# Performance work log

Hardware: AMD Instinct MI355X
Metric: run time of the kernel (lower is better)

## Reference

```python
import jax, jax.numpy as jnp
import numpy as np

B, N, DIM, H = 16, 1024, 512, 8
HEAD_DIM = DIM // H
SCALE = HEAD_DIM ** -0.5


def _dct_matrix(m):
    # Orthonormal DCT-II matrix, matching cv2.dct: D[0,:]=sqrt(1/m),
    # D[k,n]=sqrt(2/m)*cos(pi*(2n+1)*k/(2m)) for k>0.
    n = jnp.arange(m, dtype=jnp.float32)
    k = n[:, None]
    D = jnp.sqrt(2.0 / m) * jnp.cos(jnp.pi * (2.0 * n[None, :] + 1.0) * k / (2.0 * m))
    return D.at[0, :].set(jnp.sqrt(1.0 / m))


def setup_inputs() -> dict:
    key = jax.random.key(0)
    ks = jax.random.split(key, 9)
    def lin(k, fan_in, shape):
        return jax.random.normal(k, shape, jnp.float32) * (1.0 / np.sqrt(fan_in))
    return {
        "x": jax.random.normal(ks[0], (B, N, DIM), jnp.float32),
        "qkv_w": lin(ks[1], DIM, (DIM, 3 * DIM)),
        "qkv_b": lin(ks[2], DIM, (3 * DIM,)),
        "proj_w": lin(ks[3], DIM, (DIM, DIM)),
        "proj_b": lin(ks[4], DIM, (DIM,)),
        "h1_w": lin(ks[5], DIM, (DIM, DIM // 4)),
        "h1_b": jnp.zeros((DIM // 4,), jnp.float32),
        "h2_w": lin(ks[6], DIM // 4, (DIM // 4, H)),
        "h2_b": jnp.zeros((H,), jnp.float32),
        "freq_w": jnp.float32(0.5),
    }


def _extract_dct_features(x):
    # x: (B, N, C). Mirrors extract_dct_features incl. the .detach() in torch.
    B_, N_, _ = x.shape
    m = int(np.ceil(np.sqrt(N_)))  # static
    x_mean = x.mean(axis=-1)                                   # (B, N)
    A = jnp.pad(x_mean, ((0, 0), (0, m * m - N_))).reshape(B_, m, m)
    D = _dct_matrix(m)
    dct2 = jnp.einsum('km,bmn,ln->bkl', D, A, D)               # 2D DCT per sample
    dct_feat = dct2.reshape(B_, m * m)[:, :N_]
    dct_feat = jnp.clip(dct_feat, -10.0, 10.0)
    norm = jnp.linalg.norm(dct_feat, axis=1, keepdims=True) + 1e-5
    return jax.lax.stop_gradient(dct_feat / norm)              # (B, N)


def reference(x, qkv_w, qkv_b, proj_w, proj_b, h1_w, h1_b, h2_w, h2_b, freq_w):
    B_, N_, C = x.shape
    # QKV projection -> (3, B, H, N, head_dim)
    qkv = (x @ qkv_w + qkv_b).reshape(B_, N_, 3, H, C // H)
    qkv = jnp.transpose(qkv, (2, 0, 3, 1, 4))
    q, k, v = qkv[0] * SCALE, qkv[1], qkv[2]
    attn = jnp.einsum('bhnd,bhmd->bhnm', q, k)                 # (B, H, N, N)

    # Frequency-domain attention term
    dct_feat = _extract_dct_features(x)                        # (B, N)
    x_avg = x.mean(axis=1)                                     # (B, C)
    head_w = jax.nn.relu(x_avg @ h1_w + h1_b) @ h2_w + h2_b    # (B, H)
    weighted = dct_feat[:, None, :] * head_w[:, :, None]       # (B, H, N)
    freq_attn = jnp.einsum('bhn,bhm->bnm', weighted, weighted) # (B, N, N)
    row_sum = jnp.maximum(freq_attn.sum(axis=-1, keepdims=True), 1e-5)
    freq_attn = jnp.clip(freq_attn / row_sum, 0.0, 1.0)

    aw = jax.nn.sigmoid(freq_w)
    attn = (1.0 - aw) * attn + aw * freq_attn[:, None, :, :]
    attn = jax.nn.softmax(attn, axis=-1)

    out = jnp.einsum('bhnm,bhmd->bhnd', attn, v)
    out = jnp.transpose(out, (0, 2, 1, 3)).reshape(B_, N_, C)
    return out @ proj_w + proj_b
```

## Files before the change

kernel.cpp:

```cpp
#include <hip/hip_runtime.h>
#include <hip/hip_bf16.h>
#include <math.h>

#define PI_F  3.14159265358979323846f
#define LOG2E 1.44269504088896340736f

typedef __attribute__((ext_vector_type(8))) short          bf16x8;
typedef __attribute__((ext_vector_type(8))) unsigned short ushort8;
typedef __attribute__((ext_vector_type(4))) float          f32x4;

__device__ __forceinline__ unsigned short f2bf(float f) {
  union { float f; unsigned u; } v; v.f = f;
  unsigned r = v.u + 0x7fffu + ((v.u >> 16) & 1u);
  return (unsigned short)(r >> 16);
}

__device__ __forceinline__ unsigned short f2bf_hw(float f) {
  __hip_bfloat16 h = __float2bfloat16(f);
  return *reinterpret_cast<unsigned short*>(&h);
}

#define GLOAD16(g, l)                                                         \
  __builtin_amdgcn_global_load_lds(                                           \
      (const __attribute__((address_space(1))) void*)(g),                     \
      (__attribute__((address_space(3))) void*)(l), 16, 0, 0)

static const size_t OFF_XB  = 0;
static const size_t OFF_QB  = 16777216;
static const size_t OFF_KB  = 33554432;
static const size_t OFF_VT  = 67108864;
static const size_t OFF_AO  = 83886080;
static const size_t OFF_WT  = 100663296;
static const size_t OFF_PWT = 102236160;
static const size_t OFF_XM  = 102760448;
static const size_t OFF_XA  = 102825984;
static const size_t OFF_DF  = 102858752;
static const size_t OFF_CR  = 102924352;

__global__ __launch_bounds__(256) void k_xmean_cvt(const float* __restrict__ x,
                                                   float* __restrict__ xmean,
                                                   unsigned short* __restrict__ xb) {
  int row  = blockIdx.x * 4 + (threadIdx.x >> 6);
  int lane = threadIdx.x & 63;
  const float* px = x + (size_t)row * 512 + lane * 8;
  float4 a = ((const float4*)px)[0];
  float4 b = ((const float4*)px)[1];
  ushort8 o;
  o[0] = f2bf(a.x); o[1] = f2bf(a.y); o[2] = f2bf(a.z); o[3] = f2bf(a.w);
  o[4] = f2bf(b.x); o[5] = f2bf(b.y); o[6] = f2bf(b.z); o[7] = f2bf(b.w);
  *(ushort8*)(xb + (size_t)row * 512 + lane * 8) = o;
  float s = a.x + a.y + a.z + a.w + b.x + b.y + b.z + b.w;
  for (int off = 32; off; off >>= 1) s += __shfl_down(s, off);
  if (lane == 0) xmean[row] = s * (1.f / 512.f);
}

__global__ __launch_bounds__(512) void k_xavg(const unsigned short* __restrict__ xb,
                                              float* __restrict__ xavg) {
  int b = blockIdx.x, chunk = blockIdx.y;
  int c = threadIdx.x;
  const unsigned short* px = xb + ((size_t)b * 1024 + (size_t)chunk * 64) * 512 + c;
  float s = 0.f;
#pragma unroll 8
  for (int n = 0; n < 64; ++n) {
    unsigned u = (unsigned)px[(size_t)n * 512] << 16;
    s += *reinterpret_cast<float*>(&u);
  }
  atomicAdd(&xavg[b * 512 + c], s);
}

__global__ __launch_bounds__(1024) void k_dct_headw(const float* __restrict__ xmean,
                                                    const float* __restrict__ xavg,
                                                    const float* __restrict__ h1w,
                                                    const float* __restrict__ h1b,
                                                    const float* __restrict__ h2w,
                                                    const float* __restrict__ h2b,
                                                    const float* __restrict__ freqw,
                                                    float* __restrict__ dfeat,
                                                    float* __restrict__ crow) {
  __shared__ float A[32][33], Dm[32][33], Tm[32][33];
  __shared__ float red[1024];
  __shared__ float nrm, tsum_s;
  __shared__ float xa[512];
  __shared__ float part[8][128];
  __shared__ float h1s[128];
  __shared__ float hw[8];
  int b = blockIdx.x, t = threadIdx.x;
  if (t < 512) xa[t] = xavg[b * 512 + t] * (1.f / 1024.f);
  int kk = t >> 5, nn = t & 31;
  A[kk][nn] = xmean[b * 1024 + t];
  float dv = (kk == 0) ? sqrtf(1.f / 32.f)
                       : sqrtf(2.f / 32.f) * cosf(PI_F * (2.f * nn + 1.f) * (float)kk / 64.f);
  Dm[kk][nn] = dv;
  __syncthreads();
  float acc = 0.f;
  for (int m = 0; m < 32; ++m) acc += Dm[kk][m] * A[m][nn];
  Tm[kk][nn] = acc;
  __syncthreads();
  float acc2 = 0.f;
  for (int n = 0; n < 32; ++n) acc2 += Tm[kk][n] * Dm[nn][n];
  float val = fminf(fmaxf(acc2, -10.f), 10.f);
  red[t] = val * val;
  __syncthreads();
  for (int s = 512; s; s >>= 1) { if (t < s) red[t] += red[t + s]; __syncthreads(); }
  if (t == 0) nrm = sqrtf(red[0]) + 1e-5f;
  __syncthreads();
  float dn = val / nrm;
  dfeat[b * 1024 + t] = dn;
  red[t] = dn;
  __syncthreads();
  for (int s = 512; s; s >>= 1) { if (t < s) red[t] += red[t + s]; __syncthreads(); }
  if (t == 0) tsum_s = red[0];
  {
    int j = t & 127, c = t >> 7;
    float a1 = 0.f;
    const float* wcol = h1w + (size_t)c * 64 * 128 + j;
#pragma unroll 8
    for (int i = 0; i < 64; ++i) a1 += xa[c * 64 + i] * wcol[(size_t)i * 128];
    part[c][j] = a1;
  }
  __syncthreads();
  if (t < 128) {
    float a1 = h1b[t];
#pragma unroll
    for (int c = 0; c < 8; ++c) a1 += part[c][t];
    h1s[t] = fmaxf(a1, 0.f);
  }
  __syncthreads();
  if (t < 8) {
    float a2 = h2b[t];
    for (int j = 0; j < 128; ++j) a2 += h1s[j] * h2w[j * 8 + t];
    hw[t] = a2;
  }
  __syncthreads();
  float s2 = 0.f;
#pragma unroll
  for (int h = 0; h < 8; ++h) s2 += hw[h] * hw[h];
  float Tb = tsum_s;
  const float aw2 = (1.f / (1.f + __expf(-freqw[0]))) * LOG2E;
  float p = s2 * dn;
  crow[b * 1024 + t] = aw2 * p / fmaxf(p * Tb, 1e-5f);
}

__global__ __launch_bounds__(256) void k_wtrans2(const float* __restrict__ w1,
                                                 unsigned short* __restrict__ wt1,
                                                 const float* __restrict__ w2,
                                                 unsigned short* __restrict__ wt2) {
  __shared__ unsigned short T[64 * 65];
  int bx = blockIdx.x;
  const float* w;
  unsigned short* wt;
  int Nw, n0;
  if (bx < 24) { w = w1; wt = wt1; Nw = 1536; n0 = bx * 64; }
  else         { w = w2; wt = wt2; Nw = 512;  n0 = (bx - 24) * 64; }
  int k0 = blockIdx.y * 64;
  int t = threadIdx.x;
  int r = t >> 2, c0 = (t & 3) * 16;
  const float* src = w + (size_t)(k0 + r) * Nw + n0 + c0;
#pragma unroll
  for (int q = 0; q < 4; ++q) {
    float4 v4 = *(const float4*)(src + q * 4);
    T[(c0 + q * 4 + 0) * 65 + r] = f2bf(v4.x);
    T[(c0 + q * 4 + 1) * 65 + r] = f2bf(v4.y);
    T[(c0 + q * 4 + 2) * 65 + r] = f2bf(v4.z);
    T[(c0 + q * 4 + 3) * 65 + r] = f2bf(v4.w);
  }
  __syncthreads();
  int nl = t >> 2, koff = (t & 3) * 16;
  ushort8 o0, o1;
#pragma unroll
  for (int e = 0; e < 8; ++e) o0[e] = T[nl * 65 + koff + e];
#pragma unroll
  for (int e = 0; e < 8; ++e) o1[e] = T[nl * 65 + koff + 8 + e];
  unsigned short* dst = wt + (size_t)(n0 + nl) * 512 + k0 + koff;
  *(ushort8*)(dst) = o0;
  *(ushort8*)(dst + 8) = o1;
}

template <int MODE>
__global__ __launch_bounds__(256) void k_gemm(const unsigned short* __restrict__ A,
                                              const unsigned short* __restrict__ Bt,
                                              const float* __restrict__ bias,
                                              const float* __restrict__ freqw,
                                              unsigned short* __restrict__ o_q,
                                              unsigned short* __restrict__ o_k,
                                              unsigned short* __restrict__ o_vt,
                                              float* __restrict__ o_f) {
  __shared__ __align__(16) unsigned short As[128 * 64];
  __shared__ __align__(16) unsigned short Bs[128 * 64];
  const int t = threadIdx.x, w = t >> 6, l = t & 63;
  const int lg = l >> 4, ln = l & 15;
  const int wm = w >> 1, wn = w & 1;
  constexpr int NX = (MODE == 0) ? 12 : 4;
  const int bid = blockIdx.x, xcd = bid & 7, idx = bid >> 3;
  const int bx = idx % NX, by = xcd * 16 + idx / NX;
  const int row0 = by * 128, col0 = bx * 128;

  f32x4 acc[4][4];
#pragma unroll
  for (int i = 0; i < 4; ++i)
#pragma unroll
    for (int j = 0; j < 4; ++j) acc[i][j] = (f32x4){0.f, 0.f, 0.f, 0.f};

  int aoff[4][2], boff[4][2];
#pragma unroll
  for (int mt = 0; mt < 4; ++mt)
#pragma unroll
    for (int ks = 0; ks < 2; ++ks) {
      int ra = wm * 64 + mt * 16 + ln;
      aoff[mt][ks] = ra * 64 + (((lg + ks * 4) ^ (ra & 7)) << 3);
      int rb = wn * 64 + mt * 16 + ln;
      boff[mt][ks] = rb * 64 + (((lg + ks * 4) ^ (rb & 7)) << 3);
    }

  for (int k0 = 0; k0 < 512; k0 += 64) {
#pragma unroll
    for (int j = 0; j < 4; ++j) {
      int g = (j * 4 + w) * 64 + l;
      int row = g >> 3, slot = g & 7;
      int ss = slot ^ (row & 7);
      GLOAD16(A + (size_t)(row0 + row) * 512 + k0 + ss * 8, As + (size_t)(j * 4 + w) * 512);
      GLOAD16(Bt + (size_t)(col0 + row) * 512 + k0 + ss * 8, Bs + (size_t)(j * 4 + w) * 512);
    }
    __syncthreads();
#pragma unroll
    for (int ks = 0; ks < 2; ++ks) {
      bf16x8 av[4], bv[4];
#pragma unroll
      for (int mt = 0; mt < 4; ++mt) av[mt] = *(const bf16x8*)(As + aoff[mt][ks]);
#pragma unroll
      for (int nt = 0; nt < 4; ++nt) bv[nt] = *(const bf16x8*)(Bs + boff[nt][ks]);
#pragma unroll
      for (int mt = 0; mt < 4; ++mt)
#pragma unroll
        for (int nt = 0; nt < 4; ++nt)
          acc[mt][nt] = __builtin_amdgcn_mfma_f32_16x16x32_bf16(av[mt], bv[nt], acc[mt][nt], 0, 0, 0);
    }
    __syncthreads();
  }

  if (MODE == 0) {
    const int sel = col0 >> 9;
    if (sel == 2) {
      unsigned short* T = (wn == 0) ? As : Bs;
#pragma unroll
      for (int nt = 0; nt < 4; ++nt) {
        int dcol = nt * 16 + ln;
        float bcol = bias[col0 + wn * 64 + dcol];
#pragma unroll
        for (int mt = 0; mt < 4; ++mt)
#pragma unroll
          for (int r = 0; r < 4; ++r) {
            int rowL = wm * 64 + mt * 16 + lg * 4 + r;
            int slot = (rowL >> 3) ^ (dcol & 7);
            T[dcol * 128 + slot * 8 + (rowL & 7)] = f2bf(acc[mt][nt][r] + bcol);
          }
      }
      __syncthreads();
      int b_ = row0 >> 10, n0 = row0 & 1023;
      int h0 = (col0 & 511) >> 6;
      int dcol = t >> 2, rseg = (t & 3) * 32;
#pragma unroll
      for (int half = 0; half < 2; ++half) {
        const unsigned short* S = half ? Bs : As;
        size_t plane = ((size_t)(b_ * 8 + h0 + half)) << 16;
        unsigned short* dst = o_vt + plane + (size_t)dcol * 1024 + n0 + rseg;
#pragma unroll
        for (int j = 0; j < 4; ++j) {
          int slot = ((rseg >> 3) + j) ^ (dcol & 7);
          *(ushort8*)(dst + j * 8) = *(const ushort8*)(S + dcol * 128 + slot * 8);
        }
      }
      return;
    }
    unsigned short* outp = (sel == 0) ? o_q : o_k;
    const float aw = 1.f / (1.f + __expf(-freqw[0]));
    const float scl = (sel == 0) ? 0.125f * (1.f - aw) * LOG2E : 1.f;
#pragma unroll
    for (int nt = 0; nt < 4; ++nt) {
      int colg = col0 + wn * 64 + nt * 16 + ln;
      float bcol = bias[colg];
      int h = (colg >> 6) & 7, d = colg & 63;
#pragma unroll
      for (int mt = 0; mt < 4; ++mt)
#pragma unroll
        for (int r = 0; r < 4; ++r) {
          int row = row0 + wm * 64 + mt * 16 + lg * 4 + r;
          int bidx = row >> 10, n = row & 1023;
          float val = (acc[mt][nt][r] + bcol) * scl;
          outp[(((size_t)(bidx * 8 + h)) << 16) + (n << 6) + d] = f2bf(val);
        }
    }
  } else {
#pragma unroll
    for (int nt = 0; nt < 4; ++nt) {
      int colg = col0 + wn * 64 + nt * 16 + ln;
      float bcol = bias[colg];
#pragma unroll
      for (int mt = 0; mt < 4; ++mt)
#pragma unroll
        for (int r = 0; r < 4; ++r) {
          int row = row0 + wm * 64 + mt * 16 + lg * 4 + r;
          o_f[(size_t)row * 512 + colg] = acc[mt][nt][r] + bcol;
        }
    }
  }
}

__global__ __launch_bounds__(256) void k_attn(const unsigned short* __restrict__ qb,
                                              const unsigned short* __restrict__ kb,
                                              const unsigned short* __restrict__ vtg,
                                              const float* __restrict__ crow,
                                              const float* __restrict__ dfeat,
                                              const float* __restrict__ freqw,
                                              unsigned short* __restrict__ ao) {
  __shared__ __align__(16) unsigned short Ks[2][64 * 64];
  __shared__ __align__(16) unsigned short Vs[2][64 * 64];
  __shared__ __align__(16) unsigned short Ps[4][32 * 64];
  __shared__ __align__(16) float Df[1024];
  const int bid = blockIdx.x, xcd = bid & 7, idx = bid >> 3;
  const int bh = xcd * 16 + (idx >> 3), qt = idx & 7;
  const int b = bh >> 3, h = bh & 7;
  const int t = threadIdx.x, w = t >> 6, l = t & 63;
  const int lg = l >> 4, ln = l & 15;
  const size_t base = ((size_t)(b * 8 + h)) << 16;
  const float aw2 = (1.f / (1.f + __expf(-freqw[0]))) * LOG2E;

  *(float4*)(&Df[t * 4]) = *(const float4*)(dfeat + b * 1024 + t * 4);

  const int qrow0 = qt * 128 + w * 32;
  bf16x8 qf[2][2];
#pragma unroll
  for (int mt = 0; mt < 2; ++mt)
#pragma unroll
    for (int ks = 0; ks < 2; ++ks)
      qf[mt][ks] = *(const bf16x8*)(qb + base + (size_t)(qrow0 + mt * 16 + ln) * 64 + lg * 8 + ks * 32);

  float cr2[2][4];
#pragma unroll
  for (int mt = 0; mt < 2; ++mt)
#pragma unroll
    for (int r = 0; r < 4; ++r)
      cr2[mt][r] = crow[b * 1024 + qrow0 + mt * 16 + lg * 4 + r];

  f32x4 accO[2][4];
#pragma unroll
  for (int mt = 0; mt < 2; ++mt)
#pragma unroll
    for (int dt = 0; dt < 4; ++dt) accO[mt][dt] = (f32x4){0.f, 0.f, 0.f, 0.f};
  float mrow[2][4], psum[2][4];
#pragma unroll
  for (int mt = 0; mt < 2; ++mt)
#pragma unroll
    for (int r = 0; r < 4; ++r) { mrow[mt][r] = -1e30f; psum[mt][r] = 0.f; }

  int rdoff[2];
#pragma unroll
  for (int ks = 0; ks < 2; ++ks) rdoff[ks] = ln * 64 + (((lg + ks * 4) ^ (ln & 7)) << 3);
  int pwoff[4][4];
#pragma unroll
  for (int nt = 0; nt < 4; ++nt)
#pragma unroll
    for (int r = 0; r < 4; ++r) {
      int prow = lg * 4 + r;
      pwoff[nt][r] = prow * 64 + ((((nt << 1) | (ln >> 3)) ^ (prow & 7)) << 3) + (ln & 7);
    }

  const int g0 = w * 64 + l, g1 = (4 + w) * 64 + l;
  const int srow0 = g0 >> 3, sslot0 = (g0 & 7) ^ (srow0 & 7);
  const int srow1 = g1 >> 3, sslot1 = (g1 & 7) ^ (srow1 & 7);

  GLOAD16(kb + base + (size_t)srow0 * 64 + sslot0 * 8, Ks[0] + (size_t)w * 512);
  GLOAD16(vtg + base + (size_t)srow0 * 1024 + sslot0 * 8, Vs[0] + (size_t)w * 512);
  GLOAD16(kb + base + (size_t)srow1 * 64 + sslot1 * 8, Ks[0] + (size_t)(4 + w) * 512);
  GLOAD16(vtg + base + (size_t)srow1 * 1024 + sslot1 * 8, Vs[0] + (size_t)(4 + w) * 512);

  for (int kt = 0; kt < 16; ++kt) {
    const int cur = kt & 1;
    asm volatile("s_waitcnt lgkmcnt(0)" ::: "memory");
    __builtin_amdgcn_s_barrier();
    if (kt < 15) {
      const int kn = kt + 1;
      GLOAD16(kb + base + (size_t)(kn * 64 + srow0) * 64 + sslot0 * 8, Ks[cur ^ 1] + (size_t)w * 512);
      GLOAD16(vtg + base + (size_t)srow0 * 1024 + kn * 64 + sslot0 * 8, Vs[cur ^ 1] + (size_t)w * 512);
      GLOAD16(kb + base + (size_t)(kn * 64 + srow1) * 64 + sslot1 * 8, Ks[cur ^ 1] + (size_t)(4 + w) * 512);
      GLOAD16(vtg + base + (size_t)srow1 * 1024 + kn * 64 + sslot1 * 8, Vs[cur ^ 1] + (size_t)(4 + w) * 512);
      asm volatile("s_waitcnt vmcnt(4)" ::: "memory");
    } else {
      asm volatile("s_waitcnt vmcnt(0)" ::: "memory");
    }
    __builtin_amdgcn_s_barrier();

    float dmv[4];
#pragma unroll
    for (int nt = 0; nt < 4; ++nt) dmv[nt] = Df[kt * 64 + nt * 16 + ln];
    f32x4 s[2][4];
#pragma unroll
    for (int mt = 0; mt < 2; ++mt)
#pragma unroll
      for (int nt = 0; nt < 4; ++nt)
#pragma unroll
        for (int r = 0; r < 4; ++r)
          s[mt][nt][r] = __builtin_amdgcn_fmed3f(cr2[mt][r] * dmv[nt], 0.f, aw2);
    __builtin_amdgcn_s_setprio(1);
#pragma unroll
    for (int nt = 0; nt < 4; ++nt) {
      bf16x8 kf0 = *(const bf16x8*)(Ks[cur] + nt * 1024 + rdoff[0]);
      bf16x8 kf1 = *(const bf16x8*)(Ks[cur] + nt * 1024 + rdoff[1]);
#pragma unroll
      for (int mt = 0; mt < 2; ++mt) {
        s[mt][nt] = __builtin_amdgcn_mfma_f32_16x16x32_bf16(qf[mt][0], kf0, s[mt][nt], 0, 0, 0);
        s[mt][nt] = __builtin_amdgcn_mfma_f32_16x16x32_bf16(qf[mt][1], kf1, s[mt][nt], 0, 0, 0);
      }
    }
    __builtin_amdgcn_s_setprio(0);

    float lmax[2][4];
    bool viol = false;
#pragma unroll
    for (int mt = 0; mt < 2; ++mt)
#pragma unroll
      for (int r = 0; r < 4; ++r) {
        lmax[mt][r] = fmaxf(fmaxf(s[mt][0][r], s[mt][1][r]), fmaxf(s[mt][2][r], s[mt][3][r]));
        viol = viol || (lmax[mt][r] > mrow[mt][r] + 8.f);
      }
    if (__any(viol)) {
#pragma unroll
      for (int mt = 0; mt < 2; ++mt)
#pragma unroll
        for (int r = 0; r < 4; ++r) {
          float pmax = lmax[mt][r];
          pmax = fmaxf(pmax, __shfl_xor(pmax, 1));
          pmax = fmaxf(pmax, __shfl_xor(pmax, 2));
          pmax = fmaxf(pmax, __shfl_xor(pmax, 4));
          pmax = fmaxf(pmax, __shfl_xor(pmax, 8));
          float mnew = fmaxf(mrow[mt][r], pmax);
          float sc = __builtin_amdgcn_exp2f(mrow[mt][r] - mnew);
          psum[mt][r] *= sc;
          mrow[mt][r] = mnew;
#pragma unroll
          for (int dt = 0; dt < 4; ++dt) accO[mt][dt][r] *= sc;
        }
    }
#pragma unroll
    for (int mt = 0; mt < 2; ++mt)
#pragma unroll
      for (int r = 0; r < 4; ++r) {
        float p0 = __builtin_amdgcn_exp2f(s[mt][0][r] - mrow[mt][r]);
        float p1 = __builtin_amdgcn_exp2f(s[mt][1][r] - mrow[mt][r]);
        float p2 = __builtin_amdgcn_exp2f(s[mt][2][r] - mrow[mt][r]);
        float p3 = __builtin_amdgcn_exp2f(s[mt][3][r] - mrow[mt][r]);
        psum[mt][r] += (p0 + p1) + (p2 + p3);
        Ps[w][mt * 1024 + pwoff[0][r]] = f2bf_hw(p0);
        Ps[w][mt * 1024 + pwoff[1][r]] = f2bf_hw(p1);
        Ps[w][mt * 1024 + pwoff[2][r]] = f2bf_hw(p2);
        Ps[w][mt * 1024 + pwoff[3][r]] = f2bf_hw(p3);
      }

    bf16x8 pa[2][2];
#pragma unroll
    for (int mt = 0; mt < 2; ++mt)
#pragma unroll
      for (int ks = 0; ks < 2; ++ks)
        pa[mt][ks] = *(const bf16x8*)(Ps[w] + mt * 1024 + rdoff[ks]);
    __builtin_amdgcn_s_setprio(1);
#pragma unroll
    for (int dt = 0; dt < 4; ++dt) {
      bf16x8 vf0 = *(const bf16x8*)(Vs[cur] + dt * 1024 + rdoff[0]);
      bf16x8 vf1 = *(const bf16x8*)(Vs[cur] + dt * 1024 + rdoff[1]);
#pragma unroll
      for (int mt = 0; mt < 2; ++mt) {
        accO[mt][dt] = __builtin_amdgcn_mfma_f32_16x16x32_bf16(pa[mt][0], vf0, accO[mt][dt], 0, 0, 0);
        accO[mt][dt] = __builtin_amdgcn_mfma_f32_16x16x32_bf16(pa[mt][1], vf1, accO[mt][dt], 0, 0, 0);
      }
    }
    __builtin_amdgcn_s_setprio(0);
  }

#pragma unroll
  for (int mt = 0; mt < 2; ++mt)
#pragma unroll
    for (int r = 0; r < 4; ++r) {
      float lr = psum[mt][r];
      lr += __shfl_xor(lr, 1);
      lr += __shfl_xor(lr, 2);
      lr += __shfl_xor(lr, 4);
      lr += __shfl_xor(lr, 8);
      float inv = 1.f / lr;
      int n = qrow0 + mt * 16 + lg * 4 + r;
#pragma unroll
      for (int dt = 0; dt < 4; ++dt)
        ao[((size_t)(b * 1024 + n)) * 512 + h * 64 + dt * 16 + ln] = f2bf(accO[mt][dt][r] * inv);
    }
}

extern "C" void kernel_launch(void* const* d_in, const int* in_sizes, int n_in,
                              void* d_out, int out_size, void* d_ws, size_t ws_size,
                              hipStream_t stream) {
  const float* x      = (const float*)d_in[0];
  const float* qkv_w  = (const float*)d_in[1];
  const float* qkv_b  = (const float*)d_in[2];
  const float* proj_w = (const float*)d_in[3];
  const float* proj_b = (const float*)d_in[4];
  const float* h1_w   = (const float*)d_in[5];
  const float* h1_b   = (const float*)d_in[6];
  const float* h2_w   = (const float*)d_in[7];
  const float* h2_b   = (const float*)d_in[8];
  const float* freq_w = (const float*)d_in[9];

  char* ws = (char*)d_ws;
  unsigned short* xb  = (unsigned short*)(ws + OFF_XB);
  unsigned short* qbp = (unsigned short*)(ws + OFF_QB);
  unsigned short* kbp = (unsigned short*)(ws + OFF_KB);
  unsigned short* vtg = (unsigned short*)(ws + OFF_VT);
  unsigned short* ao  = (unsigned short*)(ws + OFF_AO);
  unsigned short* wt  = (unsigned short*)(ws + OFF_WT);
  unsigned short* pwt = (unsigned short*)(ws + OFF_PWT);
  float* xmean = (float*)(ws + OFF_XM);
  float* xavg  = (float*)(ws + OFF_XA);
  float* dfeat = (float*)(ws + OFF_DF);
  float* crow  = (float*)(ws + OFF_CR);
  float* out   = (float*)d_out;

  hipMemsetAsync(xavg, 0, 16 * 512 * sizeof(float), stream);

  k_xmean_cvt<<<dim3(4096), 256, 0, stream>>>(x, xmean, xb);
  k_xavg<<<dim3(16, 16), 512, 0, stream>>>(xb, xavg);
  k_wtrans2<<<dim3(32, 8), 256, 0, stream>>>(qkv_w, wt, proj_w, pwt);
  k_dct_headw<<<dim3(16), 1024, 0, stream>>>(xmean, xavg, h1_w, h1_b, h2_w, h2_b,
                                             freq_w, dfeat, crow);
  k_gemm<0><<<dim3(12 * 128), 256, 0, stream>>>(xb, wt, qkv_b, freq_w, qbp, kbp, vtg, nullptr);
  k_attn<<<dim3(1024), 256, 0, stream>>>(qbp, kbp, vtg, crow, dfeat, freq_w, ao);
  k_gemm<1><<<dim3(4 * 128), 256, 0, stream>>>(ao, pwt, proj_b, freq_w, nullptr, nullptr, nullptr, out);
}
```

Baseline: 167.9 us.

## Software-pipeline QK^T one tile ahead of softmax and PV in attention loop

Restructures the attention main loop so the QK^T MFMAs for tile kt+1 are issued before the softmax/PV work of tile kt, using two ping-pong score register sets and a two-iteration manually unrolled body. K and V loads are issued two tiles ahead with split prefetch points (K after the next QK, V after PV with an extra barrier). This aims to overlap MFMA with exp/softmax VALU work and hide global load latency, at the cost of higher register pressure and an extra barrier per iteration.

```diff
diff --git a/kernel.cpp b/kernel.cpp
--- a/kernel.cpp
+++ b/kernel.cpp
@@ -370,49 +370,75 @@
   const int srow1 = g1 >> 3, sslot1 = (g1 & 7) ^ (srow1 & 7);
 
   GLOAD16(kb + base + (size_t)srow0 * 64 + sslot0 * 8, Ks[0] + (size_t)w * 512);
+  GLOAD16(kb + base + (size_t)srow1 * 64 + sslot1 * 8, Ks[0] + (size_t)(4 + w) * 512);
   GLOAD16(vtg + base + (size_t)srow0 * 1024 + sslot0 * 8, Vs[0] + (size_t)w * 512);
-  GLOAD16(kb + base + (size_t)srow1 * 64 + sslot1 * 8, Ks[0] + (size_t)(4 + w) * 512);
   GLOAD16(vtg + base + (size_t)srow1 * 1024 + sslot1 * 8, Vs[0] + (size_t)(4 + w) * 512);
-
-  for (int kt = 0; kt < 16; ++kt) {
+  GLOAD16(kb + base + (size_t)(64 + srow0) * 64 + sslot0 * 8, Ks[1] + (size_t)w * 512);
+  GLOAD16(kb + base + (size_t)(64 + srow1) * 64 + sslot1 * 8, Ks[1] + (size_t)(4 + w) * 512);
+  GLOAD16(vtg + base + (size_t)srow0 * 1024 + 64 + sslot0 * 8, Vs[1] + (size_t)w * 512);
+  GLOAD16(vtg + base + (size_t)srow1 * 1024 + 64 + sslot1 * 8, Vs[1] + (size_t)(4 + w) * 512);
+  asm volatile("s_waitcnt vmcnt(0) lgkmcnt(0)" ::: "memory");
+  __builtin_amdgcn_s_barrier();
+
+  f32x4 sA[2][4], sB[2][4];
+
+  {
+    float dmv[4];
+#pragma unroll
+    for (int nt = 0; nt < 4; ++nt) dmv[nt] = Df[nt * 16 + ln];
+#pragma unroll
+    for (int mt = 0; mt < 2; ++mt)
+#pragma unroll
+      for (int nt = 0; nt < 4; ++nt)
+#pragma unroll
+        for (int r = 0; r < 4; ++r)
+          sA[mt][nt][r] = __builtin_amdgcn_fmed3f(cr2[mt][r] * dmv[nt], 0.f, aw2);
+#pragma unroll
+    for (int nt = 0; nt < 4; ++nt) {
+      bf16x8 kf0 = *(const bf16x8*)(Ks[0] + nt * 1024 + rdoff[0]);
+      bf16x8 kf1 = *(const bf16x8*)(Ks[0] + nt * 1024 + rdoff[1]);
+#pragma unroll
+      for (int mt = 0; mt < 2; ++mt) {
+        sA[mt][nt] = __builtin_amdgcn_mfma_f32_16x16x32_bf16(qf[mt][0], kf0, sA[mt][nt], 0, 0, 0);
+        sA[mt][nt] = __builtin_amdgcn_mfma_f32_16x16x32_bf16(qf[mt][1], kf1, sA[mt][nt], 0, 0, 0);
+      }
+    }
+  }
+
+  auto body = [&](f32x4 (&sC)[2][4], f32x4 (&sN)[2][4], const int kt) {
     const int cur = kt & 1;
-    asm volatile("s_waitcnt lgkmcnt(0)" ::: "memory");
+    if (kt == 15) { asm volatile("s_waitcnt vmcnt(0)" ::: "memory"); }
+    else          { asm volatile("s_waitcnt vmcnt(2)" ::: "memory"); }
     __builtin_amdgcn_s_barrier();
+
     if (kt < 15) {
-      const int kn = kt + 1;
-      GLOAD16(kb + base + (size_t)(kn * 64 + srow0) * 64 + sslot0 * 8, Ks[cur ^ 1] + (size_t)w * 512);
-      GLOAD16(vtg + base + (size_t)srow0 * 1024 + kn * 64 + sslot0 * 8, Vs[cur ^ 1] + (size_t)w * 512);
-      GLOAD16(kb + base + (size_t)(kn * 64 + srow1) * 64 + sslot1 * 8, Ks[cur ^ 1] + (size_t)(4 + w) * 512);
-      GLOAD16(vtg + base + (size_t)srow1 * 1024 + kn * 64 + sslot1 * 8, Vs[cur ^ 1] + (size_t)(4 + w) * 512);
-      asm volatile("s_waitcnt vmcnt(4)" ::: "memory");
-    } else {
-      asm volatile("s_waitcnt vmcnt(0)" ::: "memory");
-    }
-    __builtin_amdgcn_s_barrier();
-
-    float dmv[4];
-#pragma unroll
-    for (int nt = 0; nt < 4; ++nt) dmv[nt] = Df[kt * 64 + nt * 16 + ln];
-    f32x4 s[2][4];
-#pragma unroll
-    for (int mt = 0; mt < 2; ++mt)
-#pragma unroll
-      for (int nt = 0; nt < 4; ++nt)
-#pragma unroll
-        for (int r = 0; r < 4; ++r)
-          s[mt][nt][r] = __builtin_amdgcn_fmed3f(cr2[mt][r] * dmv[nt], 0.f, aw2);
-    __builtin_amdgcn_s_setprio(1);
-#pragma unroll
-    for (int nt = 0; nt < 4; ++nt) {
-      bf16x8 kf0 = *(const bf16x8*)(Ks[cur] + nt * 1024 + rdoff[0]);
-      bf16x8 kf1 = *(const bf16x8*)(Ks[cur] + nt * 1024 + rdoff[1]);
-#pragma unroll
-      for (int mt = 0; mt < 2; ++mt) {
-        s[mt][nt] = __builtin_amdgcn_mfma_f32_16x16x32_bf16(qf[mt][0], kf0, s[mt][nt], 0, 0, 0);
-        s[mt][nt] = __builtin_amdgcn_mfma_f32_16x16x32_bf16(qf[mt][1], kf1, s[mt][nt], 0, 0, 0);
-      }
-    }
-    __builtin_amdgcn_s_setprio(0);
+      float dmv[4];
+#pragma unroll
+      for (int nt = 0; nt < 4; ++nt) dmv[nt] = Df[(kt + 1) * 64 + nt * 16 + ln];
+#pragma unroll
+      for (int mt = 0; mt < 2; ++mt)
+#pragma unroll
+        for (int nt = 0; nt < 4; ++nt)
+#pragma unroll
+          for (int r = 0; r < 4; ++r)
+            sN[mt][nt][r] = __builtin_amdgcn_fmed3f(cr2[mt][r] * dmv[nt], 0.f, aw2);
+      __builtin_amdgcn_s_setprio(1);
+#pragma unroll
+      for (int nt = 0; nt < 4; ++nt) {
+        bf16x8 kf0 = *(const bf16x8*)(Ks[cur ^ 1] + nt * 1024 + rdoff[0]);
+        bf16x8 kf1 = *(const bf16x8*)(Ks[cur ^ 1] + nt * 1024 + rdoff[1]);
+#pragma unroll
+        for (int mt = 0; mt < 2; ++mt) {
+          sN[mt][nt] = __builtin_amdgcn_mfma_f32_16x16x32_bf16(qf[mt][0], kf0, sN[mt][nt], 0, 0, 0);
+          sN[mt][nt] = __builtin_amdgcn_mfma_f32_16x16x32_bf16(qf[mt][1], kf1, sN[mt][nt], 0, 0, 0);
+        }
+      }
+      __builtin_amdgcn_s_setprio(0);
+    }
+    if (kt < 14) {
+      GLOAD16(kb + base + (size_t)((kt + 2) * 64 + srow0) * 64 + sslot0 * 8, Ks[cur] + (size_t)w * 512);
+      GLOAD16(kb + base + (size_t)((kt + 2) * 64 + srow1) * 64 + sslot1 * 8, Ks[cur] + (size_t)(4 + w) * 512);
+    }
 
     float lmax[2][4];
     bool viol = false;
@@ -420,7 +446,7 @@
     for (int mt = 0; mt < 2; ++mt)
 #pragma unroll
       for (int r = 0; r < 4; ++r) {
-        lmax[mt][r] = fmaxf(fmaxf(s[mt][0][r], s[mt][1][r]), fmaxf(s[mt][2][r], s[mt][3][r]));
+        lmax[mt][r] = fmaxf(fmaxf(sC[mt][0][r], sC[mt][1][r]), fmaxf(sC[mt][2][r], sC[mt][3][r]));
         viol = viol || (lmax[mt][r] > mrow[mt][r] + 8.f);
       }
     if (__any(viol)) {
@@ -445,10 +471,10 @@
     for (int mt = 0; mt < 2; ++mt)
 #pragma unroll
       for (int r = 0; r < 4; ++r) {
-        float p0 = __builtin_amdgcn_exp2f(s[mt][0][r] - mrow[mt][r]);
-        float p1 = __builtin_amdgcn_exp2f(s[mt][1][r] - mrow[mt][r]);
-        float p2 = __builtin_amdgcn_exp2f(s[mt][2][r] - mrow[mt][r]);
-        float p3 = __builtin_amdgcn_exp2f(s[mt][3][r] - mrow[mt][r]);
+        float p0 = __builtin_amdgcn_exp2f(sC[mt][0][r] - mrow[mt][r]);
+        float p1 = __builtin_amdgcn_exp2f(sC[mt][1][r] - mrow[mt][r]);
+        float p2 = __builtin_amdgcn_exp2f(sC[mt][2][r] - mrow[mt][r]);
+        float p3 = __builtin_amdgcn_exp2f(sC[mt][3][r] - mrow[mt][r]);
         psum[mt][r] += (p0 + p1) + (p2 + p3);
         Ps[w][mt * 1024 + pwoff[0][r]] = f2bf_hw(p0);
         Ps[w][mt * 1024 + pwoff[1][r]] = f2bf_hw(p1);
@@ -474,6 +500,18 @@
       }
     }
     __builtin_amdgcn_s_setprio(0);
+
+    asm volatile("s_waitcnt lgkmcnt(0)" ::: "memory");
+    __builtin_amdgcn_s_barrier();
+    if (kt < 14) {
+      GLOAD16(vtg + base + (size_t)srow0 * 1024 + (kt + 2) * 64 + sslot0 * 8, Vs[cur] + (size_t)w * 512);
+      GLOAD16(vtg + base + (size_t)srow1 * 1024 + (kt + 2) * 64 + sslot1 * 8, Vs[cur] + (size_t)(4 + w) * 512);
+    }
+  };
+
+  for (int kt = 0; kt < 16; kt += 2) {
+    body(sA, sB, kt);
+    body(sB, sA, kt + 1);
   }
 
 #pragma unroll
```

Result: slower. 204.2 us (+21.6%).
